# Performance work log

Hardware: AMD Instinct MI355X
Metric: run time of the kernel (lower is better)

Reference implementation:

```python
import jax, jax.numpy as jnp
import numpy as np

TRACE_LR = 0.1
TRACE_DECAY = 0.99
ERASE_LR = 1.0
EPS = 1e-8


def setup_inputs() -> dict:
    key = jax.random.key(0)
    k1, k2, k3, k4 = jax.random.split(key, 4)
    B, H, S, D = 8, 8, 4096, 64
    DM = 768
    Q = jax.random.normal(k1, (B, H, S, D), dtype=jnp.float32)
    V = jax.random.normal(k2, (B, H, S, D), dtype=jnp.float32)
    # value_traces buffer (small random state so erase path is non-trivial)
    trace = jax.random.normal(k3, (H, D, D), dtype=jnp.float32) * 0.01
    # W_out: Linear(H*D -> DM), weight shape (DM, H*D), out = x @ W.T
    W_out = jax.random.normal(k4, (DM, H * D), dtype=jnp.float32) / np.sqrt(H * D)
    return {"Q": Q, "V": V, "trace": trace, "W_out": W_out}


def _hebbian_write(Q, V, trace):
    """Erase-before-write + decayed Hebbian outer-product update.

    Q, V: (B, H, S, D); trace: (H, D, D). Shift-1 offset: key at i, value at i+2.
    """
    B, H, S, D = Q.shape
    Q_store = Q[:, :, :-2, :]            # (B,H,S-2,D)
    V_store = V[:, :, 2:, :]             # (B,H,S-2,D)
    denom = B * (S - 2)
    # reconsolidation erasure of old associations along normalized keys
    Q_norm = jnp.clip(jnp.linalg.norm(Q_store, axis=-1, keepdims=True), EPS)
    Q_erase = Q_store / Q_norm
    V_old = jnp.einsum('bhip,hpq->bhiq', Q_erase, trace)
    erase = jnp.einsum('bhip,bhiq->hpq', Q_erase, V_old) / denom
    trace = trace - ERASE_LR * erase
    # Hebbian outer-product write
    update = jnp.einsum('bhip,bhiq->hpq', Q_store, V_store) / denom
    return TRACE_DECAY * trace + TRACE_LR * update


def reference(Q, V, trace, W_out):
    B, H, S, D = Q.shape
    new_trace = _hebbian_write(Q, V, trace)
    # shift-1 retrieval: Q_addr at position i uses Q from position i-1
    Q_addr = jnp.concatenate(
        [jnp.zeros_like(Q[:, :, :1, :]), Q[:, :, :-1, :]], axis=2)  # (B,H,S,D)
    V_ret = jnp.einsum('bhsp,hpq->bhsq', Q_addr, new_trace)          # (B,H,S,D)
    V_ret = V_ret.transpose(0, 2, 1, 3).reshape(B, S, H * D)         # (B,S,H*D)
    return V_ret @ W_out.T                                           # (B,S,d_model)
```

## Files before the change

### kernel.cpp

```cpp
#include <hip/hip_runtime.h>

#define B_ 8
#define H_ 8
#define S_ 4096
#define D_ 64
#define DM_ 768
#define NSTORE 4094
#define DENOM 32752.0f

typedef short bfrag_t __attribute__((ext_vector_type(8)));
typedef float f32x4_t __attribute__((ext_vector_type(4)));

__device__ inline unsigned short f2bf(float x) {
    unsigned int u = __float_as_uint(x);
    unsigned int r = (u + 0x7fffu + ((u >> 16) & 1u)) >> 16;
    return (unsigned short)r;
}

__device__ inline unsigned int cvtpk(float lo, float hi) {
    unsigned int r;
    asm("v_cvt_pk_bf16_f32 %0, %1, %2" : "=v"(r) : "v"(lo), "v"(hi));
    return r;
}

__device__ inline void pl16swap(float& a, float& b) {
    asm("v_permlane16_swap_b32 %0, %1" : "+v"(a), "+v"(b));
}
__device__ inline void pl32swap(float& a, float& b) {
    asm("v_permlane32_swap_b32 %0, %1" : "+v"(a), "+v"(b));
}

template <int CTRL>
__device__ inline float dpp_add(float x) {
    int y = __builtin_amdgcn_update_dpp(0, __float_as_int(x), CTRL, 0xf, 0xf, true);
    return x + __int_as_float(y);
}

__device__ inline void async_copy16(const void* g, void* lds) {
    __builtin_amdgcn_global_load_lds((__attribute__((address_space(1))) void*)g,
                                     (__attribute__((address_space(3))) void*)lds,
                                     16, 0, 0);
}

__device__ inline void barrier_lds_only() {
    __builtin_amdgcn_sched_barrier(0);
    asm volatile("s_waitcnt lgkmcnt(0)" ::: "memory");
    __builtin_amdgcn_s_barrier();
    __builtin_amdgcn_sched_barrier(0);
}

__device__ inline void barrier_vm_drain() {
    __builtin_amdgcn_sched_barrier(0);
    asm volatile("s_waitcnt vmcnt(0) lgkmcnt(0)" ::: "memory");
    __builtin_amdgcn_s_barrier();
    __builtin_amdgcn_sched_barrier(0);
}

#define MFMA16(a, b, c) __builtin_amdgcn_mfma_f32_16x16x32_bf16((a), (b), (c), 0, 0, 0)

template <bool PART>
__global__ __launch_bounds__(256, 4) void gram_kernel(
    const float* __restrict__ Q, const float* __restrict__ V,
    float* __restrict__ gG, float* __restrict__ gU,
    unsigned short* __restrict__ Qbf, float* __restrict__ gP, int writeQbf) {
    const int split = blockIdx.x, h = blockIdx.y, b = blockIdx.z;
    const int nsplit = gridDim.x;
    const int rowsPer = 4096 / nsplit;
    const int nTiles = rowsPer >> 6;
    const int tmask = nTiles - 1;
    const int t = threadIdx.x;
    const int wave = t >> 6, lane = t & 63;
    const int quad = lane >> 4, l15 = lane & 15;
    const int rgrp = t >> 4;
    const int c4 = t & 15;
    __shared__ __align__(16) unsigned short Qs[2][4096];
    __shared__ __align__(16) unsigned short Vs[2][4096];

    const size_t bh = (size_t)(b * H_ + h);
    const float* Qbh = Q + bh * S_ * D_;
    const float* Vbh = V + bh * S_ * D_;
    unsigned short* Qo = Qbf + bh * S_ * D_;

    f32x4_t accG[4] = {}, accU[4] = {};
    const int r0 = split * rowsPer;

    float4 qr[4], vr[4];
    auto loadT = [&](int tile) {
        const int rbase = r0 + tile * 64;
        #pragma unroll
        for (int i = 0; i < 4; ++i) {
            int r = rbase + i * 16 + rgrp;
            qr[i] = *(const float4*)(Qbh + (size_t)r * D_ + c4 * 4);
            vr[i] = (r < NSTORE) ? *(const float4*)(Vbh + (size_t)(r + 2) * D_ + c4 * 4)
                                 : make_float4(0.f, 0.f, 0.f, 0.f);
        }
    };
    auto rd8 = [&](const unsigned short* arr, int p, int gk) {
        const int bx = p & 15;
        uint2 lo = *(const uint2*)&arr[p * 64 + (((gk * 2) ^ bx) << 2)];
        uint2 hi = *(const uint2*)&arr[p * 64 + (((gk * 2 + 1) ^ bx) << 2)];
        union { uint2 u2[2]; bfrag_t f; } u;
        u.u2[0] = lo; u.u2[1] = hi;
        return u.f;
    };

    const int tstart = (split * 3 + h * 5 + b * 7) & tmask;

    loadT(tstart);
    for (int it = 0; it < nTiles; ++it) {
        const int tile = (tstart + it) & tmask;
        const int buf = it & 1;
        const int rbase = r0 + tile * 64;
        unsigned short* Qlds = Qs[buf];
        unsigned short* Vlds = Vs[buf];
        #pragma unroll
        for (int i = 0; i < 4; ++i) {
            int r = rbase + i * 16 + rgrp;
            float4 q4 = qr[i], v4 = vr[i];
            if (writeQbf) {
                uint2 u = make_uint2(cvtpk(q4.x, q4.y), cvtpk(q4.z, q4.w));
                *(uint2*)(Qo + (size_t)r * D_ + c4 * 4) = u;
            }
            if (r >= NSTORE) q4 = make_float4(0.f, 0.f, 0.f, 0.f);
            float ss = q4.x * q4.x + q4.y * q4.y + q4.z * q4.z + q4.w * q4.w;
            ss = dpp_add<0xB1>(ss);
            ss = dpp_add<0x4E>(ss);
            ss = dpp_add<0x141>(ss);
            ss = dpp_add<0x140>(ss);
            float sc = fmaxf(ss, 1e-16f);
            float sr = rsqrtf(sc);
            float sv = sc * sr;
            float a0 = q4.x * sr, a1 = q4.y * sr, a2 = q4.z * sr, a3 = q4.w * sr;
            float b0 = v4.x * sv, b1 = v4.y * sv, b2 = v4.z * sv, b3 = v4.w * sv;
            pl16swap(a0, a1); pl16swap(a2, a3);
            pl32swap(a0, a2); pl32swap(a1, a3);
            pl16swap(b0, b1); pl16swap(b2, b3);
            pl32swap(b0, b2); pl32swap(b1, b3);
            const int p = c4 * 4 + quad;
            const int off = p * 64 + (((i * 4 + wave) ^ (p & 15)) << 2);
            *(uint2*)&Qlds[off] = make_uint2(cvtpk(a0, a1), cvtpk(a2, a3));
            *(uint2*)&Vlds[off] = make_uint2(cvtpk(b0, b1), cvtpk(b2, b3));
        }
        if (it + 1 < nTiles) loadT((tstart + it + 1) & tmask);
        barrier_lds_only();
        #pragma unroll
        for (int c = 0; c < 2; ++c) {
            const int gk = c * 4 + quad;
            bfrag_t af = rd8(Qlds, wave * 16 + l15, gk);
            #pragma unroll
            for (int j = 0; j < 4; ++j) {
                bfrag_t bq = rd8(Qlds, j * 16 + l15, gk);
                bfrag_t bv = rd8(Vlds, j * 16 + l15, gk);
                accG[j] = MFMA16(af, bq, accG[j]);
                accU[j] = MFMA16(af, bv, accU[j]);
            }
        }
    }
    if (PART) {
        const int slab = split * 8 + b;
        float* base = gP + ((size_t)(h * 128 + slab) * 2) * 4096;
        #pragma unroll
        for (int j = 0; j < 4; ++j) {
            int coln = j * 16 + l15;
            #pragma unroll
            for (int r = 0; r < 4; ++r) {
                int row = wave * 16 + quad * 4 + r;
                base[row * 64 + coln]        = accG[j][r];
                base[4096 + row * 64 + coln] = accU[j][r];
            }
        }
    } else {
        float* gGh = gG + h * 4096;
        float* gUh = gU + h * 4096;
        #pragma unroll
        for (int j = 0; j < 4; ++j) {
            int coln = j * 16 + l15;
            #pragma unroll
            for (int r = 0; r < 4; ++r) {
                int row = wave * 16 + quad * 4 + r;
                atomicAdd(&gGh[row * 64 + coln], accG[j][r]);
                atomicAdd(&gUh[row * 64 + coln], accU[j][r]);
            }
        }
    }
}

__global__ __launch_bounds__(256) void reduce_kernel(
    const float* __restrict__ gP, float* __restrict__ gG, float* __restrict__ gU) {
    const int h = blockIdx.x, chunk = blockIdx.y, t = threadIdx.x;
    const int arr = t >> 7, idx = chunk * 128 + (t & 127);
    const float* base = gP + ((size_t)(h * 128) * 2 + arr) * 4096 + idx;
    const int slstart = ((h << 4) + (chunk << 2)) & 127;
    float s = 0.f;
    #pragma unroll 8
    for (int i = 0; i < 128; ++i) {
        int sl = (slstart + i) & 127;
        s += base[(size_t)sl * 2 * 4096];
    }
    (arr ? gU : gG)[h * 4096 + idx] = s;
}

__global__ __launch_bounds__(256) void wc_kernel(
    const float* __restrict__ gG, const float* __restrict__ gU,
    const float* __restrict__ trace, const float* __restrict__ Wout,
    unsigned short* __restrict__ WcT) {
    const int nc = blockIdx.x, h = blockIdx.y, t = threadIdx.x;
    __shared__ float Gs[64][68];
    __shared__ float Ts[64][68];
    __shared__ float TsT[64][68];
    __shared__ float WbT[64][132];
    const float* Gh = gG + h * 4096;
    const float* Uh = gU + h * 4096;
    const float* Th = trace + h * 4096;
    #pragma unroll
    for (int k = 0; k < 16; ++k) {
        int e = k * 256 + t;
        Gs[e >> 6][e & 63] = Gh[e];
        Ts[e >> 6][e & 63] = Th[e];
    }
    #pragma unroll
    for (int i = 0; i < 8; ++i) {
        int f = i * 256 + t;
        int n = f >> 4, q4 = f & 15;
        float4 w = *(const float4*)(Wout + (size_t)(nc * 128 + n) * 512 + h * 64 + q4 * 4);
        WbT[q4 * 4 + 0][n] = w.x; WbT[q4 * 4 + 1][n] = w.y;
        WbT[q4 * 4 + 2][n] = w.z; WbT[q4 * 4 + 3][n] = w.w;
    }
    __syncthreads();
    {
        const int p = t >> 2, q0 = (t & 3) * 16;
        f32x4_t acc[4] = {};
        for (int r = 0; r < 64; ++r) {
            float g = Gs[p][r];
            #pragma unroll
            for (int i = 0; i < 4; ++i) {
                f32x4_t tv = *(const f32x4_t*)&Ts[r][q0 + i * 4];
                acc[i] += g * tv;
            }
        }
        const float inv = 1.0f / DENOM;
        #pragma unroll
        for (int i = 0; i < 4; ++i) {
            f32x4_t ts = *(const f32x4_t*)&Ts[p][q0 + i * 4];
            f32x4_t uu = *(const f32x4_t*)(Uh + p * 64 + q0 + i * 4);
            f32x4_t res = 0.99f * (ts - acc[i] * inv) + (0.1f * inv) * uu;
            TsT[q0 + i * 4 + 0][p] = res[0];
            TsT[q0 + i * 4 + 1][p] = res[1];
            TsT[q0 + i * 4 + 2][p] = res[2];
            TsT[q0 + i * 4 + 3][p] = res[3];
        }
    }
    __syncthreads();
    const int n0 = (t >> 4) * 8, p0 = (t & 15) * 4;
    f32x4_t acc[8] = {};
    for (int q = 0; q < 64; ++q) {
        f32x4_t tp = *(const f32x4_t*)&TsT[q][p0];
        f32x4_t w0 = *(const f32x4_t*)&WbT[q][n0];
        f32x4_t w1 = *(const f32x4_t*)&WbT[q][n0 + 4];
        #pragma unroll
        for (int i = 0; i < 4; ++i) acc[i] += w0[i] * tp;
        #pragma unroll
        for (int i = 0; i < 4; ++i) acc[4 + i] += w1[i] * tp;
    }
    #pragma unroll
    for (int i = 0; i < 8; ++i) {
        int n = nc * 128 + n0 + i;
        ushort4 u;
        u.x = f2bf(acc[i][0]); u.y = f2bf(acc[i][1]);
        u.z = f2bf(acc[i][2]); u.w = f2bf(acc[i][3]);
        *(ushort4*)(WcT + (size_t)n * 512 + h * 64 + p0) = u;
    }
}

__global__ __launch_bounds__(256, 2) void matmul_fast(
    const unsigned short* __restrict__ Qb, const unsigned short* __restrict__ WcT,
    const unsigned short* __restrict__ zeroSrc, float* __restrict__ out) {
    const int mTile = blockIdx.x;
    const int nTile = blockIdx.y;
    const int t = threadIdx.x;
    const int wave = t >> 6, lane = t & 63;
    const int wm = wave >> 1, wn = wave & 1;
    const int quad = lane >> 4, l15 = lane & 15;
    __shared__ __align__(16) unsigned short As[2][128 * 64];
    __shared__ __align__(16) unsigned short Bs[2][128 * 64];
    const int b = mTile >> 5;
    const int s0 = (mTile & 31) * 128;
    const int nBase = nTile * 128;
    const int rl8 = lane >> 3, g = lane & 7;
    const int gs = g ^ rl8;
    f32x4_t acc[4][4] = {};
    const int hstart = (mTile * 3 + nTile * 5) & 7;

    auto stage = [&](int hh, int buf) {
        const int h = (hstart + hh) & 7;
        const unsigned short* Qbh = Qb + (size_t)(b * H_ + h) * S_ * D_;
        unsigned short* Ap = &As[buf][0];
        unsigned short* Bp = &Bs[buf][0];
        #pragma unroll
        for (int k = 0; k < 4; ++k) {
            int ch = wave * 4 + k;
            int row = ch * 8 + rl8;
            int s = s0 + row;
            const unsigned short* srcA = (s > 0)
                ? Qbh + (size_t)(s - 1) * 64 + gs * 8
                : zeroSrc + gs * 8;
            async_copy16(srcA, &Ap[ch * 512 + lane * 8]);
            async_copy16(WcT + (size_t)(nBase + row) * 512 + h * 64 + gs * 8,
                         &Bp[ch * 512 + lane * 8]);
        }
    };

    stage(0, 0);

    for (int hh = 0; hh < 8; ++hh) {
        const int buf = hh & 1;
        barrier_vm_drain();
        if (hh + 1 < 8) stage(hh + 1, buf ^ 1);
        const unsigned short* Ap = &As[buf][0];
        const unsigned short* Bp = &Bs[buf][0];
        #pragma unroll
        for (int c = 0; c < 2; ++c) {
            int gk = c * 4 + quad;
            bfrag_t af[4], bf[4];
            #pragma unroll
            for (int i = 0; i < 4; ++i) {
                int row = wm * 64 + i * 16 + l15;
                af[i] = *(const bfrag_t*)&Ap[row * 64 + ((gk ^ (row & 7)) << 3)];
            }
            #pragma unroll
            for (int j = 0; j < 4; ++j) {
                int row = wn * 64 + j * 16 + l15;
                bf[j] = *(const bfrag_t*)&Bp[row * 64 + ((gk ^ (row & 7)) << 3)];
            }
            #pragma unroll
            for (int i = 0; i < 4; ++i)
                #pragma unroll
                for (int j = 0; j < 4; ++j)
                    acc[i][j] = MFMA16(af[i], bf[j], acc[i][j]);
        }
    }
    const size_t mBase = (size_t)mTile * 128;
    #pragma unroll
    for (int i = 0; i < 4; ++i) {
        int mrow = wm * 64 + i * 16 + quad * 4;
        #pragma unroll
        for (int j = 0; j < 4; ++j) {
            int n = nBase + wn * 64 + j * 16 + l15;
            #pragma unroll
            for (int r = 0; r < 4; ++r)
                out[(mBase + mrow + r) * DM_ + n] = acc[i][j][r];
        }
    }
}

__global__ __launch_bounds__(256, 2) void matmul_f32(
    const float* __restrict__ Qf, const unsigned short* __restrict__ WcT,
    float* __restrict__ out) {
    const int mTile = blockIdx.x, nTile = blockIdx.y;
    const int t = threadIdx.x;
    const int wave = t >> 6, lane = t & 63;
    const int wm = wave >> 1, wn = wave & 1;
    const int quad = lane >> 4, l15 = lane & 15;
    __shared__ __align__(16) unsigned short As[128][72];
    __shared__ __align__(16) unsigned short Bs[128][72];
    const int b = mTile >> 5;
    const int s0 = (mTile & 31) * 128;
    const int nBase = nTile * 128;
    f32x4_t acc[4][4] = {};
    const int hstart = (mTile * 3 + nTile * 5) & 7;
    for (int hh = 0; hh < 8; ++hh) {
        const int h = (hstart + hh) & 7;
        const float* Qbh = Qf + (size_t)(b * H_ + h) * S_ * D_;
        #pragma unroll
        for (int i = 0; i < 8; ++i) {
            int f = i * 256 + t;
            int row = f >> 4, c4 = f & 15;
            int s = s0 + row;
            float4 q4 = make_float4(0.f, 0.f, 0.f, 0.f);
            if (s > 0) q4 = *(const float4*)(Qbh + (size_t)(s - 1) * D_ + c4 * 4);
            ushort4 u;
            u.x = f2bf(q4.x); u.y = f2bf(q4.y); u.z = f2bf(q4.z); u.w = f2bf(q4.w);
            *(ushort4*)(&As[row][c4 * 4]) = u;
        }
        #pragma unroll
        for (int i = 0; i < 4; ++i) {
            int f = i * 256 + t;
            int row = f >> 3, c8 = f & 7;
            uint4 w = *(const uint4*)(WcT + (size_t)(nBase + row) * 512 + h * 64 + c8 * 8);
            *(uint4*)(&Bs[row][c8 * 8]) = w;
        }
        __syncthreads();
        #pragma unroll
        for (int c = 0; c < 2; ++c) {
            int k0 = c * 32 + quad * 8;
            bfrag_t af[4], bf[4];
            #pragma unroll
            for (int i = 0; i < 4; ++i)
                af[i] = *(const bfrag_t*)(&As[wm * 64 + i * 16 + l15][k0]);
            #pragma unroll
            for (int j = 0; j < 4; ++j)
                bf[j] = *(const bfrag_t*)(&Bs[wn * 64 + j * 16 + l15][k0]);
            #pragma unroll
            for (int i = 0; i < 4; ++i)
                #pragma unroll
                for (int j = 0; j < 4; ++j)
                    acc[i][j] = MFMA16(af[i], bf[j], acc[i][j]);
        }
        __syncthreads();
    }
    const size_t mBase = (size_t)mTile * 128;
    #pragma unroll
    for (int i = 0; i < 4; ++i) {
        int mrow = wm * 64 + i * 16 + quad * 4;
        #pragma unroll
        for (int j = 0; j < 4; ++j) {
            int n = nBase + wn * 64 + j * 16 + l15;
            #pragma unroll
            for (int r = 0; r < 4; ++r)
                out[(mBase + mrow + r) * DM_ + n] = acc[i][j][r];
        }
    }
}

extern "C" void kernel_launch(void* const* d_in, const int* in_sizes, int n_in,
                              void* d_out, int out_size, void* d_ws, size_t ws_size,
                              hipStream_t stream) {
    const float* Q     = (const float*)d_in[0];
    const float* V     = (const float*)d_in[1];
    const float* trace = (const float*)d_in[2];
    const float* Wout  = (const float*)d_in[3];
    float* out = (float*)d_out;

    float* gG   = (float*)d_ws;
    float* gU   = gG + 32768;
    float* hole = gU + 32768;
    unsigned short* WcT = (unsigned short*)(hole + 32768);
    unsigned short* Qbf = WcT + 393216;
    float* gP = (float*)(Qbf + (size_t)B_ * H_ * S_ * D_);

    const size_t needQbf  = 1179648u + 33554432u;
    const size_t needFull = needQbf + 33554432u;
    const int mode = (ws_size >= needFull) ? 2 : ((ws_size >= needQbf) ? 1 : 0);

    (void)hipMemsetAsync(hole, 0, 256, stream);

    if (mode == 2) {
        gram_kernel<true><<<dim3(16, 8, 8), 256, 0, stream>>>(Q, V, gG, gU, Qbf, gP, 1);
        reduce_kernel<<<dim3(8, 32), 256, 0, stream>>>(gP, gG, gU);
    } else {
        (void)hipMemsetAsync(d_ws, 0, 2 * 32768 * sizeof(float), stream);
        gram_kernel<false><<<dim3(8, 8, 8), 256, 0, stream>>>(Q, V, gG, gU, Qbf, gP, mode >= 1);
    }
    wc_kernel<<<dim3(6, 8), 256, 0, stream>>>(gG, gU, trace, Wout, WcT);
    if (mode >= 1)
        matmul_fast<<<dim3(256, 6), 256, 0, stream>>>(Qbf, WcT,
                                                      (const unsigned short*)hole, out);
    else
        matmul_f32<<<dim3(256, 6), 256, 0, stream>>>(Q, WcT, out);
}
```

Before: 273.1 us.

## Halve K-tile in fast matmul to fit three blocks per CU, nontemporal stores

```diff
diff --git a/kernel.cpp b/kernel.cpp
--- a/kernel.cpp
+++ b/kernel.cpp
@@ -272,7 +272,7 @@
     }
 }
 
-__global__ __launch_bounds__(256, 2) void matmul_fast(
+__global__ __launch_bounds__(256, 3) void matmul_fast(
     const unsigned short* __restrict__ Qb, const unsigned short* __restrict__ WcT,
     const unsigned short* __restrict__ zeroSrc, float* __restrict__ out) {
     const int mTile = blockIdx.x;
@@ -281,63 +281,59 @@
     const int wave = t >> 6, lane = t & 63;
     const int wm = wave >> 1, wn = wave & 1;
     const int quad = lane >> 4, l15 = lane & 15;
-    __shared__ __align__(16) unsigned short As[2][128 * 64];
-    __shared__ __align__(16) unsigned short Bs[2][128 * 64];
+    __shared__ __align__(16) unsigned short As[2][128 * 32];
+    __shared__ __align__(16) unsigned short Bs[2][128 * 32];
     const int b = mTile >> 5;
     const int s0 = (mTile & 31) * 128;
     const int nBase = nTile * 128;
-    const int rl8 = lane >> 3, g = lane & 7;
-    const int gs = g ^ rl8;
     f32x4_t acc[4][4] = {};
     const int hstart = (mTile * 3 + nTile * 5) & 7;
 
-    auto stage = [&](int hh, int buf) {
-        const int h = (hstart + hh) & 7;
+    auto stage = [&](int st, int buf) {
+        const int h = (hstart + (st >> 1)) & 7;
+        const int kOff = (st & 1) * 32;
         const unsigned short* Qbh = Qb + (size_t)(b * H_ + h) * S_ * D_;
         unsigned short* Ap = &As[buf][0];
         unsigned short* Bp = &Bs[buf][0];
         #pragma unroll
-        for (int k = 0; k < 4; ++k) {
-            int ch = wave * 4 + k;
-            int row = ch * 8 + rl8;
+        for (int iter = 0; iter < 2; ++iter) {
+            int f = iter * 256 + t;
+            int row = f >> 2, g = f & 3;
+            int gs2 = g ^ (row & 3);
             int s = s0 + row;
             const unsigned short* srcA = (s > 0)
-                ? Qbh + (size_t)(s - 1) * 64 + gs * 8
-                : zeroSrc + gs * 8;
-            async_copy16(srcA, &Ap[ch * 512 + lane * 8]);
-            async_copy16(WcT + (size_t)(nBase + row) * 512 + h * 64 + gs * 8,
-                         &Bp[ch * 512 + lane * 8]);
+                ? Qbh + (size_t)(s - 1) * 64 + kOff + gs2 * 8
+                : zeroSrc + gs2 * 8;
+            async_copy16(srcA, &Ap[row * 32 + g * 8]);
+            async_copy16(WcT + (size_t)(nBase + row) * 512 + h * 64 + kOff + gs2 * 8,
+                         &Bp[row * 32 + g * 8]);
         }
     };
 
     stage(0, 0);
 
-    for (int hh = 0; hh < 8; ++hh) {
-        const int buf = hh & 1;
+    for (int st = 0; st < 16; ++st) {
+        const int buf = st & 1;
         barrier_vm_drain();
-        if (hh + 1 < 8) stage(hh + 1, buf ^ 1);
+        if (st + 1 < 16) stage(st + 1, buf ^ 1);
         const unsigned short* Ap = &As[buf][0];
         const unsigned short* Bp = &Bs[buf][0];
-        #pragma unroll
-        for (int c = 0; c < 2; ++c) {
-            int gk = c * 4 + quad;
-            bfrag_t af[4], bf[4];
-            #pragma unroll
-            for (int i = 0; i < 4; ++i) {
-                int row = wm * 64 + i * 16 + l15;
-                af[i] = *(const bfrag_t*)&Ap[row * 64 + ((gk ^ (row & 7)) << 3)];
-            }
-            #pragma unroll
-            for (int j = 0; j < 4; ++j) {
-                int row = wn * 64 + j * 16 + l15;
-                bf[j] = *(const bfrag_t*)&Bp[row * 64 + ((gk ^ (row & 7)) << 3)];
-            }
-            #pragma unroll
-            for (int i = 0; i < 4; ++i)
-                #pragma unroll
-                for (int j = 0; j < 4; ++j)
-                    acc[i][j] = MFMA16(af[i], bf[j], acc[i][j]);
-        }
+        bfrag_t af[4], bf[4];
+        #pragma unroll
+        for (int i = 0; i < 4; ++i) {
+            int row = wm * 64 + i * 16 + l15;
+            af[i] = *(const bfrag_t*)&Ap[row * 32 + ((quad ^ (row & 3)) << 3)];
+        }
+        #pragma unroll
+        for (int j = 0; j < 4; ++j) {
+            int row = wn * 64 + j * 16 + l15;
+            bf[j] = *(const bfrag_t*)&Bp[row * 32 + ((quad ^ (row & 3)) << 3)];
+        }
+        #pragma unroll
+        for (int i = 0; i < 4; ++i)
+            #pragma unroll
+            for (int j = 0; j < 4; ++j)
+                acc[i][j] = MFMA16(af[i], bf[j], acc[i][j]);
     }
     const size_t mBase = (size_t)mTile * 128;
     #pragma unroll
@@ -348,7 +344,8 @@
             int n = nBase + wn * 64 + j * 16 + l15;
             #pragma unroll
             for (int r = 0; r < 4; ++r)
-                out[(mBase + mrow + r) * DM_ + n] = acc[i][j][r];
+                __builtin_nontemporal_store(acc[i][j][r],
+                                            &out[(mBase + mrow + r) * DM_ + n]);
         }
     }
 }
```

After: 279.3 us. 1.02x slower.
